# Kernel tuning notes

Hardware: AMD Instinct MI355X
Metric: run time of the kernel (lower is better)

The kernel has to match this reference:

```python
import jax, jax.numpy as jnp
import numpy as np

N = 100000        # nodes
E = 1600000       # edges (before self loops)
IN_DIM = 128
OUT_DIM = 64
HEADS = 4
CH = OUT_DIM // HEADS   # 16 channels per head
G = 64            # graphs in batch
EPS = 1e-5        # GraphNorm eps
SLOPE = 0.2       # LeakyReLU negative slope (GATv2Conv default)


def setup_inputs() -> dict:
    key = jax.random.key(0)
    ks = jax.random.split(key, 8)
    x = jax.random.normal(ks[0], (N, IN_DIM), dtype=jnp.float32)
    edge_index = jax.random.randint(ks[1], (2, E), 0, N, dtype=jnp.int64)
    batch = jnp.sort(jax.random.randint(ks[2], (N,), 0, G, dtype=jnp.int64))
    s_in = 1.0 / np.sqrt(IN_DIM)
    # GATv2Conv params (share_weights=False): W_l for source, W_r for target
    Wl = jax.random.normal(ks[3], (IN_DIM, HEADS * CH), dtype=jnp.float32) * s_in
    Wr = jax.random.normal(ks[4], (IN_DIM, HEADS * CH), dtype=jnp.float32) * s_in
    att = jax.random.normal(ks[5], (HEADS, CH), dtype=jnp.float32) * (1.0 / np.sqrt(CH))
    conv_bias = jnp.zeros((HEADS * CH,), dtype=jnp.float32)
    # skip Linear
    skip_W = jax.random.normal(ks[6], (IN_DIM, OUT_DIM), dtype=jnp.float32) * s_in
    skip_b = jax.random.normal(ks[7], (OUT_DIM,), dtype=jnp.float32) * s_in
    # GraphNorm params (PyG init: weight=1, bias=0, mean_scale=1)
    ones = jnp.ones((OUT_DIM,), dtype=jnp.float32)
    zeros = jnp.zeros((OUT_DIM,), dtype=jnp.float32)
    return {
        "x": x, "edge_index": edge_index, "batch": batch,
        "Wl": Wl, "Wr": Wr, "att": att, "conv_bias": conv_bias,
        "skip_W": skip_W, "skip_b": skip_b,
        "bn_w": ones, "bn_b": zeros, "bn_ms": ones,
        "sn_w": ones, "sn_b": zeros, "sn_ms": ones,
    }


def _gatv2(x, Wl, Wr, att, bias, src, dst):
    n = x.shape[0]
    xl = (x @ Wl).reshape(n, HEADS, CH)   # source transform (also the message)
    xr = (x @ Wr).reshape(n, HEADS, CH)   # target transform
    # GATv2: score = a . LeakyReLU(xl[j] + xr[i]) per head
    e = jax.nn.leaky_relu(xl[src] + xr[dst], SLOPE)          # [E,H,C]
    score = jnp.einsum('ehc,hc->eh', e, att)                  # [E,H]
    # segment softmax over edges sharing a target node
    smax = jax.ops.segment_max(score, dst, num_segments=n)    # [N,H]
    ex = jnp.exp(score - smax[dst])
    denom = jax.ops.segment_sum(ex, dst, num_segments=n)
    alpha = ex / denom[dst]                                   # [E,H]
    out = jax.ops.segment_sum(xl[src] * alpha[:, :, None], dst, num_segments=n)
    return out.reshape(n, HEADS * CH) + bias


def _graph_norm(x, w, b, ms, batch):
    cnt = jax.ops.segment_sum(jnp.ones((x.shape[0],), x.dtype), batch, num_segments=G)
    cnt = jnp.maximum(cnt, 1.0)[:, None]
    mean = jax.ops.segment_sum(x, batch, num_segments=G) / cnt
    cen = x - mean[batch] * ms
    var = jax.ops.segment_sum(cen * cen, batch, num_segments=G) / cnt
    inv = jax.lax.rsqrt(var + EPS)
    return w * cen * inv[batch] + b


def reference(x, edge_index, batch, Wl, Wr, att, conv_bias, skip_W, skip_b,
              bn_w, bn_b, bn_ms, sn_w, sn_b, sn_ms):
    n = x.shape[0]
    loop = jnp.arange(n, dtype=edge_index.dtype)  # add_self_loops=True default
    src = jnp.concatenate([edge_index[0], loop])
    dst = jnp.concatenate([edge_index[1], loop])
    x_main = _gatv2(x, Wl, Wr, att, conv_bias, src, dst)
    x_main = _graph_norm(x_main, bn_w, bn_b, bn_ms, batch)
    x_skip = _graph_norm(x @ skip_W + skip_b, sn_w, sn_b, sn_ms, batch)
    return jax.nn.elu(x_main + x_skip)
```

## Files before the change

kernel.cpp:

```cpp
#include <hip/hip_runtime.h>

#define IND 128
#define OUTD 64
#define NG 64
#define NPART 8
#define NSTRIPE 256
#define SLOPE 0.2f
#define EPSV 1e-5f
#define JMASK 131071
#define DEGCAP 48

typedef short bf16x8 __attribute__((ext_vector_type(8)));
typedef float f32x4 __attribute__((ext_vector_type(4)));
typedef float f32x2 __attribute__((ext_vector_type(2)));

__device__ __forceinline__ unsigned bf16rne(float f) {
  unsigned u = __float_as_uint(f);
  return (u + 0x7fffu + ((u >> 16) & 1u)) >> 16;
}
__device__ __forceinline__ unsigned pack2(float a, float b) {
  return bf16rne(a) | (bf16rne(b) << 16);
}
__device__ __forceinline__ unsigned pack2u(unsigned a, unsigned b) {
  return pack2(__uint_as_float(a), __uint_as_float(b));
}

__device__ __forceinline__ void gload_lds16(const void* g, void* l) {
  __builtin_amdgcn_global_load_lds(
      (const __attribute__((address_space(1))) void*)g,
      (__attribute__((address_space(3))) void*)l, 16, 0, 0);
}

__global__ __launch_bounds__(256) void wcvt_kernel(
    const float* __restrict__ Wl, const float* __restrict__ Wr,
    const float* __restrict__ Ws, unsigned short* __restrict__ wt) {
  int i = blockIdx.x * 256 + threadIdx.x;
  if (i >= 3 * 64 * 128) return;
  int k = i & 127, col = (i >> 7) & 63, which = i >> 13;
  const float* W = (which == 0) ? Wl : (which == 1) ? Wr : Ws;
  int row = which * 64 + col;
  int t = row >> 4, m = row & 15;
  int kc = k >> 5, quad = (k >> 3) & 3, j = k & 7;
  int slot = ((t * 4 + kc) * 4 + quad) * 16 + m;
  wt[slot * 8 + j] = (unsigned short)bf16rne(W[k * OUTD + col]);
}

__device__ __forceinline__ void gemm3_body(
    int bx, const float* __restrict__ x, const unsigned short* __restrict__ wt,
    const float* __restrict__ skip_b,
    unsigned* __restrict__ xlb, float* __restrict__ xr, float* __restrict__ xs,
    int n, uint4* ldsx) {
  int tid = threadIdx.x;
  int wave = tid >> 6, lane = tid & 63;
  int m = lane & 15, quad = lane >> 4;

#pragma unroll
  for (int i = 0; i < 8; ++i) {
    int c = i * 256 + tid;
    int row = c >> 5, u = c & 31;
    int us = u ^ (row & 7);
    int growc = min(bx * 64 + row, n - 1);
    gload_lds16(x + (size_t)growc * IND + us * 4, &ldsx[c]);
  }
  __syncthreads();

  int lbase = (wave * 16 + m) * 32;
  int swz = m & 7;
  union { uint4 u; bf16x8 v; } af[4];
#pragma unroll
  for (int kc = 0; kc < 4; ++kc) {
    int u0 = kc * 8 + quad * 2;
    uint4 A0 = ldsx[lbase + (u0 ^ swz)];
    uint4 A1 = ldsx[lbase + ((u0 + 1) ^ swz)];
    af[kc].u = make_uint4(pack2u(A0.x, A0.y), pack2u(A0.z, A0.w),
                          pack2u(A1.x, A1.y), pack2u(A1.z, A1.w));
  }

  f32x4 acc[12] = {};
#pragma unroll
  for (int kc = 0; kc < 4; ++kc) {
#pragma unroll
    for (int t = 0; t < 12; ++t) {
      const bf16x8* bp =
          (const bf16x8*)&wt[(((t * 4 + kc) * 4 + quad) * 16 + m) * 8];
      acc[t] = __builtin_amdgcn_mfma_f32_16x16x32_bf16(af[kc].v, *bp, acc[t], 0, 0, 0);
    }
  }

  float sbv[4];
#pragma unroll
  for (int q = 0; q < 4; ++q) sbv[q] = skip_b[q * 16 + m];

  int orow_base = bx * 64 + wave * 16 + quad * 4;
#pragma unroll
  for (int r = 0; r < 4; ++r) {
    int orow = orow_base + r;
    bool ok = orow < n;
#pragma unroll
    for (int t = 0; t < 4; ++t) {
      float v = acc[t][r];
      float pv = __shfl_xor(v, 1);
      if (ok && !(m & 1))
        xlb[(orow << 5) + t * 8 + (m >> 1)] = pack2(v, pv);
    }
#pragma unroll
    for (int t = 4; t < 8; ++t)
      if (ok) xr[(orow << 6) + (t - 4) * 16 + m] = acc[t][r];
#pragma unroll
    for (int t = 8; t < 12; ++t)
      if (ok) xs[(orow << 6) + (t - 8) * 16 + m] = acc[t][r] + sbv[t - 8];
  }
}

__device__ __forceinline__ void scat1(int d, int s, int lo, int hi,
                                      int* count, int* __restrict__ bucket) {
  if (d >= lo && d < hi) {
    int p = atomicAdd(&count[d], 1);
    if (p < DEGCAP) bucket[d * DEGCAP + p] = s;
  }
}

__device__ __forceinline__ void scatter_body(int r, int stripe,
                                             const int* __restrict__ src,
                                             const int* __restrict__ dst,
                                             int* count, int* __restrict__ bucket,
                                             int E, int n8) {
  int lo = r * n8, hi = lo + n8;
  int per = (((E + NSTRIPE - 1) / NSTRIPE) + 3) & ~3;
  int s0 = stripe * per;
  int s1 = min(E, s0 + per);
  for (int e = s0 + (int)threadIdx.x * 4; e < s1; e += 1024) {
    if (e + 4 <= s1) {
      int4 d4 = *(const int4*)&dst[e];
      int4 s4 = *(const int4*)&src[e];
      scat1(d4.x, s4.x, lo, hi, count, bucket);
      scat1(d4.y, s4.y, lo, hi, count, bucket);
      scat1(d4.z, s4.z, lo, hi, count, bucket);
      scat1(d4.w, s4.w, lo, hi, count, bucket);
    } else {
      for (int q = e; q < s1; ++q)
        scat1(dst[q], src[q], lo, hi, count, bucket);
    }
  }
}

__device__ __forceinline__ void goff_body(int bx, const int* __restrict__ batch,
                                          int* goff, int n) {
  int i = bx * 256 + threadIdx.x;
  if (i >= n) return;
  int b = batch[i];
  int prev = (i == 0) ? -1 : batch[i - 1];
  for (int g = prev + 1; g <= b; ++g) goff[g] = i;
  if (i == n - 1)
    for (int g = b + 1; g <= NG; ++g) goff[g] = n;
}

__global__ __launch_bounds__(256) void mega1_kernel(
    const float* __restrict__ x, const unsigned short* __restrict__ wt,
    const float* __restrict__ skip_b,
    unsigned* __restrict__ xlb, float* __restrict__ xr, float* __restrict__ xs,
    const int* __restrict__ src, const int* __restrict__ dst,
    int* count, int* bucket,
    const int* __restrict__ batch, int* goff,
    int n, int E, int n8, int nbG, int nbB, int SG, int GG) {
  __shared__ uint4 ldsx[2048];
  int group = blockIdx.x >> 3, pos = blockIdx.x & 7;
  int mn = min(SG, GG), m2 = 2 * mn;
  bool isS;
  int sub;
  if (group < m2) { isS = ((group & 1) == 0); sub = group >> 1; }
  else           { isS = (SG > GG);           sub = mn + (group - m2); }
  if (isS) {
    scatter_body(pos, sub, src, dst, count, bucket, E, n8);
  } else {
    int g = sub * 8 + pos;
    if (g < nbG) gemm3_body(g, x, wt, skip_b, xlb, xr, xs, n, ldsx);
    else if (g < nbG + nbB) goff_body(g - nbG, batch, goff, n);
  }
}

__global__ __launch_bounds__(256) void edge_kernel(
    const unsigned* __restrict__ xlb, const float* __restrict__ xr,
    const int* __restrict__ count, const int* __restrict__ bucket,
    const float* __restrict__ att, const float* __restrict__ conv_bias,
    float* __restrict__ out_main, int n) {
  int tid = threadIdx.x;
  int wave = tid >> 6;
  int lane = tid & 63;
  int half = lane >> 5;
  int sub = lane & 31;
  int bx = (int)blockIdx.x;
  int node = bx * 8 + wave * 2 + half;
  bool act = node < n;
  int nodec = min(node, n - 1);
  int base2 = (nodec << 6) | (sub << 1);

  f32x2 xrc = __builtin_nontemporal_load((const f32x2*)&xr[base2]);
  unsigned us = xlb[(nodec << 5) | sub];
  float xs0 = __uint_as_float(us << 16);
  float xs1 = __uint_as_float(us & 0xffff0000u);
  float2 att2 = *(const float2*)&att[sub << 1];

  float t0 = xs0 + xrc.x, t1 = xs1 + xrc.y;
  t0 = fmaxf(t0, SLOPE * t0);
  t1 = fmaxf(t1, SLOPE * t1);
  float s = t0 * att2.x + t1 * att2.y;
  s += __shfl_xor(s, 1);
  s += __shfl_xor(s, 2);
  s += __shfl_xor(s, 4);
  const float sself = s;

  int e0 = nodec * DEGCAP;
  int deg = min(count[nodec], DEGCAP);
  int iters = max(deg, __shfl_xor(deg, 32));

  float denom = 1.f;
  float a0 = xs0, a1 = xs1;
  int i = 0;
  for (; i + 7 < iters; i += 8) {
    float p[8], v0[8], v1[8];
#pragma unroll
    for (int k = 0; k < 8; ++k) {
      bool a = (i + k < deg);
      int e = a ? (e0 + i + k) : e0;
      int j = bucket[e] & JMASK;
      unsigned u = xlb[(j << 5) | sub];
      v0[k] = __uint_as_float(u << 16);
      v1[k] = __uint_as_float(u & 0xffff0000u);
      float tx = v0[k] + xrc.x, ty = v1[k] + xrc.y;
      tx = fmaxf(tx, SLOPE * tx); ty = fmaxf(ty, SLOPE * ty);
      float sc = tx * att2.x + ty * att2.y;
      sc += __shfl_xor(sc, 1);
      sc += __shfl_xor(sc, 2);
      sc += __shfl_xor(sc, 4);
      p[k] = a ? __expf(sc - sself) : 0.f;
    }
#pragma unroll
    for (int k = 0; k < 8; ++k) {
      denom += p[k];
      a0 += p[k] * v0[k];
      a1 += p[k] * v1[k];
    }
  }
  for (; i < iters; ++i) {
    bool a = (i < deg);
    int e = a ? (e0 + i) : e0;
    int j = bucket[e] & JMASK;
    unsigned u = xlb[(j << 5) | sub];
    float v0 = __uint_as_float(u << 16);
    float v1 = __uint_as_float(u & 0xffff0000u);
    float tx = v0 + xrc.x, ty = v1 + xrc.y;
    tx = fmaxf(tx, SLOPE * tx); ty = fmaxf(ty, SLOPE * ty);
    float sc = tx * att2.x + ty * att2.y;
    sc += __shfl_xor(sc, 1);
    sc += __shfl_xor(sc, 2);
    sc += __shfl_xor(sc, 4);
    float p = a ? __expf(sc - sself) : 0.f;
    denom += p;
    a0 += p * v0;
    a1 += p * v1;
  }
  float inv = 1.f / denom;
  float2 cb = *(const float2*)&conv_bias[sub << 1];
  if (act) {
    f32x2 o; o.x = a0 * inv + cb.x; o.y = a1 * inv + cb.y;
    __builtin_nontemporal_store(o, (f32x2*)&out_main[base2]);
  }
}

__global__ __launch_bounds__(256) void stats_part_kernel(
    const float* __restrict__ mainv, const float* __restrict__ xs,
    const int* __restrict__ goff, float* __restrict__ part) {
  int g = blockIdx.x, q = blockIdx.y;
  int start = goff[g], end = goff[g + 1];
  int col = threadIdx.x & 63, grp = threadIdx.x >> 6;
  float s1m = 0.f, s2m = 0.f, s1s = 0.f, s2s = 0.f;
  for (int node = start + q * 4 + grp; node < end; node += 4 * NPART) {
    float vm = __builtin_nontemporal_load(&mainv[(node << 6) | col]);
    float vs = __builtin_nontemporal_load(&xs[(node << 6) | col]);
    s1m += vm; s2m += vm * vm;
    s1s += vs; s2s += vs * vs;
  }
  __shared__ float red[4][4][64];
  red[0][grp][col] = s1m; red[1][grp][col] = s2m;
  red[2][grp][col] = s1s; red[3][grp][col] = s2s;
  __syncthreads();
  if (threadIdx.x < 64) {
    int c = threadIdx.x;
    float* dst = &part[(g * NPART + q) * 256];
#pragma unroll
    for (int st = 0; st < 4; ++st) {
      float s = red[st][0][c] + red[st][1][c] + red[st][2][c] + red[st][3][c];
      dst[st * 64 + c] = s;
    }
  }
}

__global__ void stats_comb_kernel(
    const float* __restrict__ part, const int* __restrict__ goff,
    const float* __restrict__ bn_w, const float* __restrict__ bn_b,
    const float* __restrict__ bn_ms,
    const float* __restrict__ sn_w, const float* __restrict__ sn_b,
    const float* __restrict__ sn_ms,
    float* __restrict__ Am, float* __restrict__ Bm,
    float* __restrict__ As, float* __restrict__ Bs) {
  int g = blockIdx.x;
  int c = threadIdx.x;
  float S1m = 0.f, S2m = 0.f, S1s = 0.f, S2s = 0.f;
  for (int q = 0; q < NPART; ++q) {
    const float* p = &part[(g * NPART + q) * 256];
    S1m += p[c];       S2m += p[64 + c];
    S1s += p[128 + c]; S2s += p[192 + c];
  }
  float cnt = fmaxf((float)(goff[g + 1] - goff[g]), 1.f);
  float meanM = S1m / cnt;
  float aM = meanM * bn_ms[c];
  float varM = S2m / cnt - 2.f * aM * meanM + aM * aM;
  float invM = rsqrtf(varM + EPSV);
  float am = bn_w[c] * invM;
  Am[g * OUTD + c] = am;
  Bm[g * OUTD + c] = bn_b[c] - am * aM;
  float meanS = S1s / cnt;
  float aS = meanS * sn_ms[c];
  float varS = S2s / cnt - 2.f * aS * meanS + aS * aS;
  float invS = rsqrtf(varS + EPSV);
  float as_ = sn_w[c] * invS;
  As[g * OUTD + c] = as_;
  Bs[g * OUTD + c] = sn_b[c] - as_ * aS;
}

__global__ __launch_bounds__(256) void final_kernel(
    const float* __restrict__ xs, const int* __restrict__ batch,
    const float* __restrict__ Am, const float* __restrict__ Bm,
    const float* __restrict__ As, const float* __restrict__ Bs,
    float* out, int n) {
  int idx = blockIdx.x * 256 + threadIdx.x;
  if (idx >= n * 16) return;
  int node = idx >> 4;
  int c4 = (idx & 15) << 2;
  int g = batch[node];
  f32x4 mv = __builtin_nontemporal_load((const f32x4*)&out[idx << 2]);
  f32x4 sv = __builtin_nontemporal_load((const f32x4*)&xs[idx << 2]);
  f32x4 A1 = *(const f32x4*)&Am[g * OUTD + c4];
  f32x4 B1 = *(const f32x4*)&Bm[g * OUTD + c4];
  f32x4 A2 = *(const f32x4*)&As[g * OUTD + c4];
  f32x4 B2 = *(const f32x4*)&Bs[g * OUTD + c4];
  f32x4 v;
  v.x = A1.x * mv.x + B1.x + A2.x * sv.x + B2.x;
  v.y = A1.y * mv.y + B1.y + A2.y * sv.y + B2.y;
  v.z = A1.z * mv.z + B1.z + A2.z * sv.z + B2.z;
  v.w = A1.w * mv.w + B1.w + A2.w * sv.w + B2.w;
  v.x = (v.x > 0.f) ? v.x : (__expf(v.x) - 1.f);
  v.y = (v.y > 0.f) ? v.y : (__expf(v.y) - 1.f);
  v.z = (v.z > 0.f) ? v.z : (__expf(v.z) - 1.f);
  v.w = (v.w > 0.f) ? v.w : (__expf(v.w) - 1.f);
  __builtin_nontemporal_store(v, (f32x4*)&out[idx << 2]);
}

extern "C" void kernel_launch(void* const* d_in, const int* in_sizes, int n_in,
                              void* d_out, int out_size, void* d_ws, size_t ws_size,
                              hipStream_t stream) {
  const float* x        = (const float*)d_in[0];
  const int*   ei       = (const int*)d_in[1];
  const int*   batch    = (const int*)d_in[2];
  const float* Wl       = (const float*)d_in[3];
  const float* Wr       = (const float*)d_in[4];
  const float* att      = (const float*)d_in[5];
  const float* conv_b   = (const float*)d_in[6];
  const float* skip_W   = (const float*)d_in[7];
  const float* skip_b   = (const float*)d_in[8];
  const float* bn_w     = (const float*)d_in[9];
  const float* bn_b     = (const float*)d_in[10];
  const float* bn_ms    = (const float*)d_in[11];
  const float* sn_w     = (const float*)d_in[12];
  const float* sn_b     = (const float*)d_in[13];
  const float* sn_ms    = (const float*)d_in[14];

  int n = in_sizes[0] / IND;
  int E = in_sizes[1] / 2;
  const int* src = ei;
  const int* dst = ei + E;
  float* out = (float*)d_out;

  char* w = (char*)d_ws;
  int* count  = (int*)w;   w += (size_t)(n + 64) * 4;
  int* goff   = (int*)w;   w += (size_t)(NG + 64) * 4;
  float* Am   = (float*)w; w += (size_t)NG * OUTD * 4;
  float* Bm   = (float*)w; w += (size_t)NG * OUTD * 4;
  float* As   = (float*)w; w += (size_t)NG * OUTD * 4;
  float* Bs   = (float*)w; w += (size_t)NG * OUTD * 4;
  float* part = (float*)w; w += (size_t)NG * NPART * 256 * 4;
  unsigned short* wt = (unsigned short*)w; w += (size_t)3 * 64 * IND * 2;
  int* bucket = (int*)w;   w += (size_t)n * DEGCAP * 4;
  unsigned* xlb = (unsigned*)w; w += (size_t)n * 32 * 4;
  float* xr   = (float*)w; w += (size_t)n * OUTD * 4;
  float* xs   = (float*)w; w += (size_t)n * OUTD * 4;

  int n8 = (n + 7) / 8;
  int nbG = (n + 63) / 64;
  int nbB = (n + 255) / 256;
  int SG = NSTRIPE;
  int GG = (nbG + nbB + 7) / 8;

  (void)hipMemsetAsync(count, 0, (size_t)(n + 1) * 4, stream);

  wcvt_kernel<<<(3 * 64 * IND + 255) / 256, 256, 0, stream>>>(Wl, Wr, skip_W, wt);

  mega1_kernel<<<8 * (SG + GG), 256, 0, stream>>>(
      x, wt, skip_b, xlb, xr, xs, src, dst, count, bucket, batch, goff,
      n, E, n8, nbG, nbB, SG, GG);

  edge_kernel<<<(n + 7) / 8, 256, 0, stream>>>(xlb, xr, count, bucket, att, conv_b,
                                               out, n);
  dim3 sg(NG, NPART);
  stats_part_kernel<<<sg, 256, 0, stream>>>(out, xs, goff, part);
  stats_comb_kernel<<<NG, 64, 0, stream>>>(part, goff, bn_w, bn_b, bn_ms,
                                           sn_w, sn_b, sn_ms, Am, Bm, As, Bs);
  final_kernel<<<(n * 16 + 255) / 256, 256, 0, stream>>>(xs, batch, Am, Bm, As, Bs,
                                                         out, n);
}
```

Before: 327.2 us.

## Move skip-branch stats into edge kernel and interleave scatter/GEMM blocks evenly

The skip-path GraphNorm partial sums (xs mean and square) are computed by extra blocks prepended to the edge kernel grid, so stats_part only reads the main output. Their reads of xs overlap with the edge gather work instead of running in the serial stats pass. The mega1 block assignment also switches from strict alternation to a proportional interleave of scatter and GEMM groups. This adds divergent block roles inside edge_kernel and makes the edge kernel's grid slightly larger.

```diff
diff --git a/kernel.cpp b/kernel.cpp
--- a/kernel.cpp
+++ b/kernel.cpp
@@ -9,6 +9,7 @@
 #define EPSV 1e-5f
 #define JMASK 131071
 #define DEGCAP 48
+#define NSB (NG * NPART)
 
 typedef short bf16x8 __attribute__((ext_vector_type(8)));
 typedef float f32x4 __attribute__((ext_vector_type(4)));
@@ -165,15 +166,13 @@
     int n, int E, int n8, int nbG, int nbB, int SG, int GG) {
   __shared__ uint4 ldsx[2048];
   int group = blockIdx.x >> 3, pos = blockIdx.x & 7;
-  int mn = min(SG, GG), m2 = 2 * mn;
-  bool isS;
-  int sub;
-  if (group < m2) { isS = ((group & 1) == 0); sub = group >> 1; }
-  else           { isS = (SG > GG);           sub = mn + (group - m2); }
-  if (isS) {
-    scatter_body(pos, sub, src, dst, count, bucket, E, n8);
+  int gtot = SG + GG;
+  int before = (int)(((long long)group * SG) / gtot);
+  int after  = (int)(((long long)(group + 1) * SG) / gtot);
+  if (after > before) {
+    scatter_body(pos, before, src, dst, count, bucket, E, n8);
   } else {
-    int g = sub * 8 + pos;
+    int g = (group - before) * 8 + pos;
     if (g < nbG) gemm3_body(g, x, wt, skip_b, xlb, xr, xs, n, ldsx);
     else if (g < nbG + nbB) goff_body(g - nbG, batch, goff, n);
   }
@@ -183,13 +182,41 @@
     const unsigned* __restrict__ xlb, const float* __restrict__ xr,
     const int* __restrict__ count, const int* __restrict__ bucket,
     const float* __restrict__ att, const float* __restrict__ conv_bias,
+    const float* __restrict__ xs, const int* __restrict__ goff,
+    float* __restrict__ part,
     float* __restrict__ out_main, int n) {
   int tid = threadIdx.x;
+  int bxr = (int)blockIdx.x;
+
+  if (bxr < NSB) {
+    int g = bxr >> 3, q = bxr & 7;
+    int start = goff[g], end = goff[g + 1];
+    int col = tid & 63, grp = tid >> 6;
+    float s1s = 0.f, s2s = 0.f;
+    for (int node = start + q * 4 + grp; node < end; node += 4 * NPART) {
+      float vs = __builtin_nontemporal_load(&xs[(node << 6) | col]);
+      s1s += vs; s2s += vs * vs;
+    }
+    __shared__ float red[2][4][64];
+    red[0][grp][col] = s1s; red[1][grp][col] = s2s;
+    __syncthreads();
+    if (tid < 64) {
+      float* dstp = &part[(g * NPART + q) * 256 + 128];
+#pragma unroll
+      for (int st = 0; st < 2; ++st) {
+        float s = red[st][0][tid] + red[st][1][tid] + red[st][2][tid] +
+                  red[st][3][tid];
+        dstp[st * 64 + tid] = s;
+      }
+    }
+    return;
+  }
+
+  int bx = bxr - NSB;
   int wave = tid >> 6;
   int lane = tid & 63;
   int half = lane >> 5;
   int sub = lane & 31;
-  int bx = (int)blockIdx.x;
   int node = bx * 8 + wave * 2 + half;
   bool act = node < n;
   int nodec = min(node, n - 1);
@@ -269,27 +296,24 @@
 }
 
 __global__ __launch_bounds__(256) void stats_part_kernel(
-    const float* __restrict__ mainv, const float* __restrict__ xs,
+    const float* __restrict__ mainv,
     const int* __restrict__ goff, float* __restrict__ part) {
   int g = blockIdx.x, q = blockIdx.y;
   int start = goff[g], end = goff[g + 1];
   int col = threadIdx.x & 63, grp = threadIdx.x >> 6;
-  float s1m = 0.f, s2m = 0.f, s1s = 0.f, s2s = 0.f;
+  float s1m = 0.f, s2m = 0.f;
   for (int node = start + q * 4 + grp; node < end; node += 4 * NPART) {
     float vm = __builtin_nontemporal_load(&mainv[(node << 6) | col]);
-    float vs = __builtin_nontemporal_load(&xs[(node << 6) | col]);
     s1m += vm; s2m += vm * vm;
-    s1s += vs; s2s += vs * vs;
-  }
-  __shared__ float red[4][4][64];
+  }
+  __shared__ float red[2][4][64];
   red[0][grp][col] = s1m; red[1][grp][col] = s2m;
-  red[2][grp][col] = s1s; red[3][grp][col] = s2s;
   __syncthreads();
   if (threadIdx.x < 64) {
     int c = threadIdx.x;
     float* dst = &part[(g * NPART + q) * 256];
 #pragma unroll
-    for (int st = 0; st < 4; ++st) {
+    for (int st = 0; st < 2; ++st) {
       float s = red[st][0][c] + red[st][1][c] + red[st][2][c] + red[st][3][c];
       dst[st * 64 + c] = s;
     }
@@ -410,10 +434,11 @@
       x, wt, skip_b, xlb, xr, xs, src, dst, count, bucket, batch, goff,
       n, E, n8, nbG, nbB, SG, GG);
 
-  edge_kernel<<<(n + 7) / 8, 256, 0, stream>>>(xlb, xr, count, bucket, att, conv_b,
-                                               out, n);
+  edge_kernel<<<NSB + (n + 7) / 8, 256, 0, stream>>>(
+      xlb, xr, count, bucket, att, conv_b, xs, goff, part, out, n);
+
   dim3 sg(NG, NPART);
-  stats_part_kernel<<<sg, 256, 0, stream>>>(out, xs, goff, part);
+  stats_part_kernel<<<sg, 256, 0, stream>>>(out, goff, part);
   stats_comb_kernel<<<NG, 64, 0, stream>>>(part, goff, bn_w, bn_b, bn_ms,
                                            sn_w, sn_b, sn_ms, Am, Bm, As, Bs);
   final_kernel<<<(n * 16 + 255) / 256, 256, 0, stream>>>(xs, batch, Am, Bm, As, Bs,
```

Result: no change. 320.8 us (-1.9%).
